# Kernel optimization log

Measured on AMD Instinct MI355X. Metric: run time of the kernel, lower is better.

Reference implementation:

```python
import jax, jax.numpy as jnp
import numpy as np

N, E, B, O = 100000, 1600000, 256, 32
D, H, OD = 128, 128, 32  # node_features, hidden_dim, order_encoding_dim
L = 3  # num_layers


def setup_inputs() -> dict:
    key = jax.random.key(0)
    ks = jax.random.split(key, 32)
    g = lambda k, s, fan: jax.random.normal(k, s, jnp.float32) * (1.0 / np.sqrt(fan))
    inp = {
        'x': jax.random.normal(ks[0], (N, D), jnp.float32),
        'edge_index': jax.random.randint(ks[1], (2, E), 0, N),
        'orders': jax.random.normal(ks[2], (B, O, OD), jnp.float32),
        'batch': jnp.sort(jax.random.randint(ks[3], (N,), 0, B)),
        # GIN layers (input_dim == hidden_dim so all 3 layers stack): MLP = Lin(H,H)->ReLU->Lin(H,H), then BatchNorm1d
        'gW1': g(ks[4], (L, H, H), H), 'gb1': jnp.zeros((L, H)),
        'gW2': g(ks[5], (L, H, H), H), 'gb2': jnp.zeros((L, H)),
        'gamma': jnp.ones((L, H)), 'beta': jnp.zeros((L, H)),
        # order encoder: Lin(OD,H)->ReLU->Lin(H,H)
        'oW1': g(ks[6], (OD, H), OD), 'ob1': jnp.zeros((H,)),
        'oW2': g(ks[7], (H, H), H), 'ob2': jnp.zeros((H,)),
        # score head: Lin(4H,H)->ReLU->Lin(H,H//2)->ReLU->Lin(H//2,1)
        'sW1': g(ks[8], (4 * H, H), 4 * H), 'sb1': jnp.zeros((H,)),
        'sW2': g(ks[9], (H, H // 2), H), 'sb2': jnp.zeros((H // 2,)),
        'sW3': g(ks[10], (H // 2, 1), H // 2), 'sb3': jnp.zeros((1,)),
    }
    return inp


def reference(x, edge_index, orders, batch, gW1, gb1, gW2, gb2, gamma, beta,
              oW1, ob1, oW2, ob2, sW1, sb1, sW2, sb2, sW3, sb3):
    n = x.shape[0]
    src, dst = edge_index[0], edge_index[1]
    h = x
    nl = gW1.shape[0]
    for i in range(nl):  # fixed small layer count
        agg = jax.ops.segment_sum(h[src], dst, num_segments=n)  # sum aggregation
        z = agg + h  # (1 + eps) * x with eps = 0 (GINConv default)
        z = jnp.maximum(z @ gW1[i] + gb1[i], 0) @ gW2[i] + gb2[i]
        mu = z.mean(0)
        var = z.var(0)  # biased var, as torch BN uses for normalization
        z = (z - mu) * jax.lax.rsqrt(var + 1e-5) * gamma[i] + beta[i]
        h = jnp.maximum(z, 0) if i < nl - 1 else z  # dropout inactive (eval)
    b = orders.shape[0]
    cnt = jax.ops.segment_sum(jnp.ones((n,), h.dtype), batch, num_segments=b)
    ssum = jax.ops.segment_sum(h, batch, num_segments=b)
    smean = ssum / jnp.maximum(cnt, 1)[:, None]
    smax = jax.ops.segment_max(h, batch, num_segments=b)
    smax = jnp.where(jnp.isfinite(smax), smax, 0)
    graph = jnp.concatenate([smean, smax, ssum], axis=-1)  # [B, 3H]
    # batched over num_orders (equivalent to the python per-order loop)
    oe = jnp.maximum(orders @ oW1 + ob1, 0) @ oW2 + ob2  # [B, O, H]
    comb = jnp.concatenate(
        [jnp.broadcast_to(graph[:, None, :], (b, orders.shape[1], graph.shape[-1])), oe], axis=-1)
    s = jnp.maximum(comb @ sW1 + sb1, 0)
    s = jnp.maximum(s @ sW2 + sb2, 0)
    s = (s @ sW3 + sb3)[..., 0]  # [B, O]
    return s
```

## Files before the change

### kernel.cpp

```cpp
#include <hip/hip_runtime.h>

static constexpr int NN = 100000;
static constexpr int NE = 1600000;
static constexpr int NB = 256;
static constexpr int NO = 32;
static constexpr int HD = 128;
static constexpr long NH = (long)NN * HD;

static constexpr int BSHIFT = 9;
static constexpr int BSIZE = 1 << BSHIFT;
static constexpr int NBUCK = 256;
static constexpr int BCAP = 10240;
static constexpr int CHUNK = 16384;
static constexpr int NCHUNK = (NE + CHUNK - 1) / CHUNK;
static constexpr int POOL_ROWS = 64;
static constexpr int POOL_GRID = (NN + POOL_ROWS - 1) / POOL_ROWS;
static constexpr int NSUB = 64;
static constexpr int GATHER_GRID = NN / 4;
static constexpr int FL_ROWS = 32;
static constexpr int FL_GRID = (NN + FL_ROWS - 1) / FL_ROWS;

typedef _Float16 f16x8 __attribute__((ext_vector_type(8)));
typedef _Float16 f16x4 __attribute__((ext_vector_type(4)));
typedef _Float16 f16x2 __attribute__((ext_vector_type(2)));
typedef float f32x4 __attribute__((ext_vector_type(4)));

__device__ __forceinline__ unsigned int encf(float f) {
  unsigned int u = __float_as_uint(f);
  return (u & 0x80000000u) ? ~u : (u | 0x80000000u);
}
__device__ __forceinline__ float decf(unsigned int e) {
  return (e & 0x80000000u) ? __uint_as_float(e & 0x7fffffffu) : __uint_as_float(~e);
}

__global__ void bucket_scatter(const int* __restrict__ ei, int* __restrict__ cursor,
                               unsigned int* __restrict__ binned) {
  __shared__ int cnt[NBUCK];
  __shared__ int runbase[NBUCK];
  const int t = threadIdx.x;
  cnt[t] = 0;
  __syncthreads();
  long start = (long)blockIdx.x * CHUNK;
  long end = min((long)NE, start + CHUNK);
  for (long e = start + t; e < end; e += 256)
    atomicAdd(&cnt[ei[NE + e] >> BSHIFT], 1);
  __syncthreads();
  int c = cnt[t];
  runbase[t] = c ? atomicAdd(&cursor[t], c) : 0;
  cnt[t] = 0;
  __syncthreads();
  for (long e = start + t; e < end; e += 256) {
    int d = ei[NE + e], s = ei[e];
    int b = d >> BSHIFT;
    int pos = b * BCAP + runbase[b] + atomicAdd(&cnt[b], 1);
    binned[pos] = ((unsigned int)s << BSHIFT) | (unsigned int)(d & (BSIZE - 1));
  }
}

__global__ void bucket_csr(const unsigned int* __restrict__ binned,
                           const int* __restrict__ cursor,
                           int* __restrict__ rowStart, int* __restrict__ rowEnd,
                           int* __restrict__ col) {
  __shared__ int cnt[BSIZE];
  __shared__ int excl[BSIZE];
  __shared__ int cur[BSIZE];
  __shared__ int part[256];
  const int b = blockIdx.x;
  const int t = threadIdx.x;
  const int lo = b * BCAP;
  const int hi = lo + cursor[b];
  cnt[t] = 0; cnt[t + 256] = 0;
  __syncthreads();
  for (int i = lo + t; i < hi; i += 256)
    atomicAdd(&cnt[binned[i] & (BSIZE - 1)], 1);
  __syncthreads();
  int a0 = cnt[2 * t], a1 = cnt[2 * t + 1];
  int s = a0 + a1;
  part[t] = s;
  __syncthreads();
  for (int off = 1; off < 256; off <<= 1) {
    int u = (t >= off) ? part[t - off] : 0;
    __syncthreads();
    part[t] += u;
    __syncthreads();
  }
  int ebase = part[t] - s;
  excl[2 * t] = ebase;
  excl[2 * t + 1] = ebase + a0;
  __syncthreads();
  const int node0 = b * BSIZE;
  for (int i = t; i < BSIZE; i += 256) {
    int node = node0 + i;
    if (node < NN) {
      rowStart[node] = lo + excl[i];
      rowEnd[node]   = lo + excl[i] + cnt[i];
    }
    cur[i] = lo + excl[i];
  }
  __syncthreads();
  for (int i = lo + t; i < hi; i += 256) {
    unsigned int v = binned[i];
    int pos = atomicAdd(&cur[v & (BSIZE - 1)], 1);
    col[pos] = (int)(v >> BSHIFT);
  }
}

__global__ void f32to16_kernel(const float* __restrict__ in, _Float16* __restrict__ out) {
  long i = (long)(blockIdx.x * 256 + threadIdx.x) * 8;
  if (i >= NH) return;
  float4 a = *reinterpret_cast<const float4*>(in + i);
  float4 b = *reinterpret_cast<const float4*>(in + i + 4);
  f16x8 v;
  v[0] = (_Float16)a.x; v[1] = (_Float16)a.y; v[2] = (_Float16)a.z; v[3] = (_Float16)a.w;
  v[4] = (_Float16)b.x; v[5] = (_Float16)b.y; v[6] = (_Float16)b.z; v[7] = (_Float16)b.w;
  *reinterpret_cast<f16x8*>(out + i) = v;
}

__global__ void pack_w_kernel(const float* __restrict__ gW1, const float* __restrict__ gW2,
                              _Float16* __restrict__ Wp) {
  int tid = blockIdx.x * blockDim.x + threadIdx.x;
  if (tid >= 12288) return;
  int lane = tid & 63;
  int s = (tid >> 6) & 3;
  int t = (tid >> 8) & 7;
  int which = (tid >> 11) & 1;
  int layer = tid >> 12;
  const float* W = (which ? gW2 : gW1) + (long)layer * 128 * 128;
  _Float16* dst = Wp + (long)tid * 8;
  int kbase = s * 32 + ((lane >> 4) << 3);
  int n = t * 16 + (lane & 15);
#pragma unroll
  for (int j = 0; j < 8; ++j) dst[j] = (_Float16)W[(kbase + j) * 128 + n];
}

__global__ void pack_head_kernel(const float* __restrict__ oW1, const float* __restrict__ oW2,
                                 const float* __restrict__ sW1, const float* __restrict__ sW2,
                                 _Float16* __restrict__ dst) {
  int tid = blockIdx.x * blockDim.x + threadIdx.x;
  if (tid >= 5632) return;
  const float* W; int K, N, rowOff;
  int base = tid;
  if (tid < 512)       { W = oW1; K = 32;  N = 128; rowOff = 0;   }
  else if (tid < 2560) { W = oW2; K = 128; N = 128; rowOff = 0;   base = tid - 512; }
  else if (tid < 4608) { W = sW1; K = 128; N = 128; rowOff = 384; base = tid - 2560; }
  else                 { W = sW2; K = 128; N = 64;  rowOff = 0;   base = tid - 4608; }
  int lane = base & 63;
  int fs = base >> 6;
  int NS = K >> 5;
  int s = fs % NS;
  int tt = fs / NS;
  int k = s * 32 + ((lane >> 4) << 3);
  int n = tt * 16 + (lane & 15);
  _Float16* d = dst + (long)tid * 8;
#pragma unroll
  for (int j = 0; j < 8; ++j) d[j] = (_Float16)W[(long)(rowOff + k + j) * N + n];
}

__global__ void gather_kernel(const _Float16* __restrict__ hin, const int* __restrict__ rowStart,
                              const int* __restrict__ rowEnd, const int* __restrict__ col,
                              _Float16* __restrict__ z) {
  const int node = (blockIdx.x * blockDim.x + threadIdx.x) >> 6;
  if (node >= NN) return;
  const int c2 = (threadIdx.x & 63) * 2;
  auto ldh = [&](int n) -> float2 {
    f16x2 h = *reinterpret_cast<const f16x2*>(hin + (long)n * HD + c2);
    return make_float2((float)h[0], (float)h[1]);
  };
  const int lo = rowStart[node];
  const int hi = rowEnd[node];
  float2 acc = ldh(node);
  int j = lo;
  for (; j + 4 <= hi; j += 4) {
    int s0 = col[j], s1 = col[j + 1], s2 = col[j + 2], s3 = col[j + 3];
    float2 v0 = ldh(s0), v1 = ldh(s1), v2 = ldh(s2), v3 = ldh(s3);
    acc.x += (v0.x + v1.x) + (v2.x + v3.x);
    acc.y += (v0.y + v1.y) + (v2.y + v3.y);
  }
  if (j < hi) {
    int last = hi - 1;
    int s0 = col[j];
    int s1 = col[min(j + 1, last)];
    int s2 = col[min(j + 2, last)];
    int s3 = col[min(j + 3, last)];
    float m1 = (j + 1 < hi) ? 1.f : 0.f;
    float m2 = (j + 2 < hi) ? 1.f : 0.f;
    float m3 = (j + 3 < hi) ? 1.f : 0.f;
    float2 v0 = ldh(s0), v1 = ldh(s1), v2 = ldh(s2), v3 = ldh(s3);
    acc.x += v0.x + m1 * v1.x + m2 * v2.x + m3 * v3.x;
    acc.y += v0.y + m1 * v1.y + m2 * v2.y + m3 * v3.y;
  }
  f16x2 o;
  o[0] = (_Float16)acc.x;
  o[1] = (_Float16)acc.y;
  *reinterpret_cast<f16x2*>(z + (long)node * HD + c2) = o;
}

__global__ void __launch_bounds__(128)
fused_layer(const _Float16* __restrict__ Z, const _Float16* __restrict__ Wp,
            const float* __restrict__ b1, const float* __restrict__ b2,
            _Float16* __restrict__ Z2, float* __restrict__ accum2) {
  __shared__ _Float16 Abuf[FL_ROWS * 136];
  __shared__ float red[256];
  const int t = threadIdx.x;
  const int row0 = blockIdx.x * FL_ROWS;
  const int lane = t & 63;
  const int w = t >> 6;
  const int l15 = lane & 15;
  const int kgrp = lane >> 4;

  for (int idx = t; idx < FL_ROWS * 16; idx += 128) {
    int r = idx >> 4;
    int c8 = (idx & 15) * 8;
    int row = row0 + r;
    f16x8 v = {};
    if (row < NN) v = *reinterpret_cast<const f16x8*>(Z + (long)row * HD + c8);
    *reinterpret_cast<f16x8*>(&Abuf[r * 136 + c8]) = v;
  }
  red[t] = 0.f;
  red[t + 128] = 0.f;
  __syncthreads();

  f32x4 acc[8];
  {
    f16x8 af[4];
#pragma unroll
    for (int s = 0; s < 4; ++s)
      af[s] = *reinterpret_cast<const f16x8*>(&Abuf[(w * 16 + l15) * 136 + s * 32 + kgrp * 8]);
    const _Float16* W1p = Wp;
#pragma unroll
    for (int tt = 0; tt < 8; ++tt) {
      float bb = b1[tt * 16 + l15];
      acc[tt] = (f32x4){bb, bb, bb, bb};
#pragma unroll
      for (int s = 0; s < 4; ++s) {
        f16x8 bf = *reinterpret_cast<const f16x8*>(W1p + ((tt * 4 + s) * 64 + lane) * 8);
        acc[tt] = __builtin_amdgcn_mfma_f32_16x16x32_f16(af[s], bf, acc[tt], 0, 0, 0);
      }
    }
  }
#pragma unroll
  for (int tt = 0; tt < 8; ++tt) {
#pragma unroll
    for (int j = 0; j < 4; ++j) {
      float v = fmaxf(acc[tt][j], 0.f);
      Abuf[(w * 16 + kgrp * 4 + j) * 136 + tt * 16 + l15] = (_Float16)v;
    }
  }
  {
    f16x8 af[4];
#pragma unroll
    for (int s = 0; s < 4; ++s)
      af[s] = *reinterpret_cast<const f16x8*>(&Abuf[(w * 16 + l15) * 136 + s * 32 + kgrp * 8]);
    const _Float16* W2p = Wp + 16384;
#pragma unroll
    for (int tt = 0; tt < 8; ++tt) {
      float bb = b2[tt * 16 + l15];
      acc[tt] = (f32x4){bb, bb, bb, bb};
#pragma unroll
      for (int s = 0; s < 4; ++s) {
        f16x8 bf = *reinterpret_cast<const f16x8*>(W2p + ((tt * 4 + s) * 64 + lane) * 8);
        acc[tt] = __builtin_amdgcn_mfma_f32_16x16x32_f16(af[s], bf, acc[tt], 0, 0, 0);
      }
    }
  }
#pragma unroll
  for (int tt = 0; tt < 8; ++tt) {
    int c = tt * 16 + l15;
    float s = 0.f, q = 0.f;
#pragma unroll
    for (int j = 0; j < 4; ++j) {
      int r = row0 + w * 16 + kgrp * 4 + j;
      float v = acc[tt][j];
      if (r < NN) { s += v; q += v * v; }
      Abuf[(w * 16 + kgrp * 4 + j) * 136 + c] = (_Float16)v;
    }
    atomicAdd(&red[c], s);
    atomicAdd(&red[128 + c], q);
  }
  for (int idx = lane; idx < 16 * 16; idx += 64) {
    int r = w * 16 + (idx >> 4);
    int c8 = (idx & 15) * 8;
    int row = row0 + r;
    if (row < NN)
      *reinterpret_cast<f16x8*>(Z2 + (long)row * HD + c8) =
          *reinterpret_cast<const f16x8*>(&Abuf[r * 136 + c8]);
  }
  __syncthreads();
  atomicAdd(&accum2[(blockIdx.x & (NSUB - 1)) * 256 + t], red[t]);
  atomicAdd(&accum2[(blockIdx.x & (NSUB - 1)) * 256 + t + 128], red[t + 128]);
}

__global__ void bn_reduce(float* __restrict__ accum2, const float* __restrict__ gamma,
                          const float* __restrict__ beta, float* __restrict__ scsh) {
  const int c = threadIdx.x;
  float s = 0.f;
  for (int i = 0; i < NSUB; ++i) {
    s += accum2[i * 256 + c];
    accum2[i * 256 + c] = 0.f;
  }
  __shared__ float red[256];
  red[c] = s;
  __syncthreads();
  if (c < 128) {
    const float n = (float)NN;
    float mu = red[c] / n;
    float var = red[128 + c] / n - mu * mu;
    float sc = rsqrtf(var + 1e-5f) * gamma[c];
    scsh[c] = sc;
    scsh[128 + c] = beta[c] - mu * sc;
  }
}

__global__ void bn_apply(const _Float16* __restrict__ z2, const float* __restrict__ scsh,
                         _Float16* __restrict__ hn) {
  long idx = (long)blockIdx.x * 256 + threadIdx.x;
  if (idx >= (long)NN * 16) return;
  int c8 = ((int)idx & 15) * 8;
  float4 sc0 = *reinterpret_cast<const float4*>(scsh + c8);
  float4 sc1 = *reinterpret_cast<const float4*>(scsh + c8 + 4);
  float4 sh0 = *reinterpret_cast<const float4*>(scsh + 128 + c8);
  float4 sh1 = *reinterpret_cast<const float4*>(scsh + 128 + c8 + 4);
  f16x8 v = *reinterpret_cast<const f16x8*>(z2 + idx * 8);
  f16x8 o;
  o[0] = (_Float16)fmaxf(fmaf((float)v[0], sc0.x, sh0.x), 0.f);
  o[1] = (_Float16)fmaxf(fmaf((float)v[1], sc0.y, sh0.y), 0.f);
  o[2] = (_Float16)fmaxf(fmaf((float)v[2], sc0.z, sh0.z), 0.f);
  o[3] = (_Float16)fmaxf(fmaf((float)v[3], sc0.w, sh0.w), 0.f);
  o[4] = (_Float16)fmaxf(fmaf((float)v[4], sc1.x, sh1.x), 0.f);
  o[5] = (_Float16)fmaxf(fmaf((float)v[5], sc1.y, sh1.y), 0.f);
  o[6] = (_Float16)fmaxf(fmaf((float)v[6], sc1.z, sh1.z), 0.f);
  o[7] = (_Float16)fmaxf(fmaf((float)v[7], sc1.w, sh1.w), 0.f);
  *reinterpret_cast<f16x8*>(hn + idx * 8) = o;
}

__global__ void pool_init(float* __restrict__ ssum, unsigned int* __restrict__ smaxU) {
  int i = blockIdx.x * 256 + threadIdx.x;
  ssum[i] = 0.f;
  smaxU[i] = 0x007FFFFFu;
}

__global__ void pool_partial(const _Float16* __restrict__ z2, const float* __restrict__ scsh,
                             const int* __restrict__ batch,
                             float* __restrict__ ssum, unsigned int* __restrict__ smaxU) {
  const int c = threadIdx.x;
  const int row0 = blockIdx.x * POOL_ROWS;
  const int rowEnd = min(row0 + POOL_ROWS, NN);
  const float sc = scsh[c];
  const float sh = scsh[128 + c];

  int curb = batch[row0];
  float s = 0.f, m = -INFINITY;
  for (int row = row0; row < rowEnd; ++row) {
    int b = batch[row];
    if (b != curb) {
      atomicAdd(&ssum[curb * HD + c], s);
      atomicMax(&smaxU[curb * HD + c], encf(m));
      s = 0.f; m = -INFINITY; curb = b;
    }
    float v = fmaf((float)z2[(long)row * HD + c], sc, sh);
    s += v;
    m = fmaxf(m, v);
  }
  atomicAdd(&ssum[curb * HD + c], s);
  atomicMax(&smaxU[curb * HD + c], encf(m));
}

__global__ void pool_gpart(const int* __restrict__ batch, const float* __restrict__ ssum,
                           const unsigned int* __restrict__ smaxU, const float* __restrict__ sW1,
                           const float* __restrict__ sb1, float* __restrict__ gpart) {
  __shared__ float sm[128], sx[128], ss[128];
  const int b = blockIdx.x;
  const int c = threadIdx.x;
  int lo = 0, hi = NN;
  while (lo < hi) { int mid = (lo + hi) >> 1; if (batch[mid] < b) lo = mid + 1; else hi = mid; }
  const int start = lo;
  hi = NN;
  while (lo < hi) { int mid = (lo + hi) >> 1; if (batch[mid] < b + 1) lo = mid + 1; else hi = mid; }
  const int cnt = lo - start;
  float s = ssum[b * HD + c];
  sm[c] = s / fmaxf((float)cnt, 1.f);
  sx[c] = (cnt > 0) ? decf(smaxU[b * HD + c]) : 0.f;
  ss[c] = s;
  __syncthreads();
  float acc = sb1[c];
  for (int k = 0; k < 128; ++k) acc = fmaf(sm[k], sW1[k * 128 + c], acc);
  for (int k = 0; k < 128; ++k) acc = fmaf(sx[k], sW1[(128 + k) * 128 + c], acc);
  for (int k = 0; k < 128; ++k) acc = fmaf(ss[k], sW1[(256 + k) * 128 + c], acc);
  gpart[b * HD + c] = acc;
}

__global__ void __launch_bounds__(128)
head_mfma(const float* __restrict__ orders, const _Float16* __restrict__ Wh,
          const float* __restrict__ ob1, const float* __restrict__ ob2,
          const float* __restrict__ gpart, const float* __restrict__ sb2,
          const float* __restrict__ sW3, const float* __restrict__ sb3,
          float* __restrict__ out) {
  __shared__ _Float16 B1[32 * 136];
  __shared__ _Float16 B2[32 * 136];
  const int t = threadIdx.x;
  const int g = blockIdx.x;
  const int row0 = g * 32;
  const int lane = t & 63;
  const int w = t >> 6;
  const int l15 = lane & 15;
  const int kgrp = lane >> 4;
  const _Float16* oW1p  = Wh;
  const _Float16* oW2p  = Wh + 4096;
  const _Float16* sW1bp = Wh + 20480;
  const _Float16* sW2p  = Wh + 36864;

  for (int idx = t; idx < 32 * 8; idx += 128) {
    int r = idx >> 3;
    int c4 = (idx & 7) * 4;
    float4 v = *reinterpret_cast<const float4*>(orders + (long)(row0 + r) * 32 + c4);
    f16x4 h;
    h[0] = (_Float16)v.x; h[1] = (_Float16)v.y; h[2] = (_Float16)v.z; h[3] = (_Float16)v.w;
    *reinterpret_cast<f16x4*>(&B1[r * 136 + c4]) = h;
  }
  __syncthreads();

  f32x4 acc[8];
  {
    f16x8 a0 = *reinterpret_cast<const f16x8*>(&B1[(w * 16 + l15) * 136 + kgrp * 8]);
#pragma unroll
    for (int tt = 0; tt < 8; ++tt) {
      float bb = ob1[tt * 16 + l15];
      acc[tt] = (f32x4){bb, bb, bb, bb};
      f16x8 bf = *reinterpret_cast<const f16x8*>(oW1p + (tt * 64 + lane) * 8);
      acc[tt] = __builtin_amdgcn_mfma_f32_16x16x32_f16(a0, bf, acc[tt], 0, 0, 0);
    }
#pragma unroll
    for (int tt = 0; tt < 8; ++tt)
#pragma unroll
      for (int j = 0; j < 4; ++j)
        B2[(w * 16 + kgrp * 4 + j) * 136 + tt * 16 + l15] = (_Float16)fmaxf(acc[tt][j], 0.f);
  }
  {
    f16x8 af[4];
#pragma unroll
    for (int s = 0; s < 4; ++s)
      af[s] = *reinterpret_cast<const f16x8*>(&B2[(w * 16 + l15) * 136 + s * 32 + kgrp * 8]);
#pragma unroll
    for (int tt = 0; tt < 8; ++tt) {
      float bb = ob2[tt * 16 + l15];
      acc[tt] = (f32x4){bb, bb, bb, bb};
#pragma unroll
      for (int s = 0; s < 4; ++s) {
        f16x8 bf = *reinterpret_cast<const f16x8*>(oW2p + ((tt * 4 + s) * 64 + lane) * 8);
        acc[tt] = __builtin_amdgcn_mfma_f32_16x16x32_f16(af[s], bf, acc[tt], 0, 0, 0);
      }
    }
#pragma unroll
    for (int tt = 0; tt < 8; ++tt)
#pragma unroll
      for (int j = 0; j < 4; ++j)
        B1[(w * 16 + kgrp * 4 + j) * 136 + tt * 16 + l15] = (_Float16)acc[tt][j];
  }
  {
    f16x8 af[4];
#pragma unroll
    for (int s = 0; s < 4; ++s)
      af[s] = *reinterpret_cast<const f16x8*>(&B1[(w * 16 + l15) * 136 + s * 32 + kgrp * 8]);
#pragma unroll
    for (int tt = 0; tt < 8; ++tt) {
      acc[tt] = (f32x4){0.f, 0.f, 0.f, 0.f};
#pragma unroll
      for (int s = 0; s < 4; ++s) {
        f16x8 bf = *reinterpret_cast<const f16x8*>(sW1bp + ((tt * 4 + s) * 64 + lane) * 8);
        acc[tt] = __builtin_amdgcn_mfma_f32_16x16x32_f16(af[s], bf, acc[tt], 0, 0, 0);
      }
    }
#pragma unroll
    for (int tt = 0; tt < 8; ++tt) {
      int c = tt * 16 + l15;
      float gp = gpart[g * HD + c];
#pragma unroll
      for (int j = 0; j < 4; ++j)
        B2[(w * 16 + kgrp * 4 + j) * 136 + c] = (_Float16)fmaxf(acc[tt][j] + gp, 0.f);
    }
  }
  {
    f16x8 af[4];
#pragma unroll
    for (int s = 0; s < 4; ++s)
      af[s] = *reinterpret_cast<const f16x8*>(&B2[(w * 16 + l15) * 136 + s * 32 + kgrp * 8]);
#pragma unroll
    for (int tt = 0; tt < 4; ++tt) {
      float bb = sb2[tt * 16 + l15];
      acc[tt] = (f32x4){bb, bb, bb, bb};
#pragma unroll
      for (int s = 0; s < 4; ++s) {
        f16x8 bf = *reinterpret_cast<const f16x8*>(sW2p + ((tt * 4 + s) * 64 + lane) * 8);
        acc[tt] = __builtin_amdgcn_mfma_f32_16x16x32_f16(af[s], bf, acc[tt], 0, 0, 0);
      }
    }
    float rsum[4] = {0.f, 0.f, 0.f, 0.f};
#pragma unroll
    for (int tt = 0; tt < 4; ++tt) {
      float wv = sW3[tt * 16 + l15];
#pragma unroll
      for (int j = 0; j < 4; ++j)
        rsum[j] = fmaf(fmaxf(acc[tt][j], 0.f), wv, rsum[j]);
    }
#pragma unroll
    for (int j = 0; j < 4; ++j) {
      rsum[j] += __shfl_xor(rsum[j], 1);
      rsum[j] += __shfl_xor(rsum[j], 2);
      rsum[j] += __shfl_xor(rsum[j], 4);
      rsum[j] += __shfl_xor(rsum[j], 8);
    }
    if (l15 == 0) {
      float b3 = sb3[0];
#pragma unroll
      for (int j = 0; j < 4; ++j)
        out[row0 + w * 16 + kgrp * 4 + j] = rsum[j] + b3;
    }
  }
}

extern "C" void kernel_launch(void* const* d_in, const int* in_sizes, int n_in,
                              void* d_out, int out_size, void* d_ws, size_t ws_size,
                              hipStream_t stream) {
  const float* x      = (const float*)d_in[0];
  const int*   ei     = (const int*)d_in[1];
  const float* orders = (const float*)d_in[2];
  const int*   batch  = (const int*)d_in[3];
  const float* gW1    = (const float*)d_in[4];
  const float* gb1    = (const float*)d_in[5];
  const float* gW2    = (const float*)d_in[6];
  const float* gb2    = (const float*)d_in[7];
  const float* gamma  = (const float*)d_in[8];
  const float* beta   = (const float*)d_in[9];
  const float* oW1    = (const float*)d_in[10];
  const float* ob1    = (const float*)d_in[11];
  const float* oW2    = (const float*)d_in[12];
  const float* ob2    = (const float*)d_in[13];
  const float* sW1    = (const float*)d_in[14];
  const float* sb1    = (const float*)d_in[15];
  const float* sW2    = (const float*)d_in[16];
  const float* sb2    = (const float*)d_in[17];
  const float* sW3    = (const float*)d_in[18];
  const float* sb3    = (const float*)d_in[19];
  float* out = (float*)d_out;

  char* ws = (char*)d_ws;
  _Float16* xh    = (_Float16*)ws;
  _Float16* bufAh = xh + NH;
  _Float16* bufCh = bufAh + NH;
  float* accum2 = (float*)(bufCh + NH);
  float* scsh   = accum2 + NSUB * 256;
  float* ssum   = scsh + 256;
  unsigned int* smaxU = (unsigned int*)(ssum + NB * HD);
  float* gpart = (float*)(smaxU + NB * HD);
  int* rowStart = (int*)(gpart + NB * HD);
  int* rowEnd   = rowStart + NN;
  int* col      = rowEnd + NN;
  unsigned int* binned = (unsigned int*)(col + NBUCK * BCAP);
  int* cursor = (int*)(binned + NBUCK * BCAP);
  _Float16* Wp  = (_Float16*)(cursor + NBUCK);
  _Float16* Wh  = Wp + 3 * 32768;

  hipMemsetAsync(cursor, 0, NBUCK * sizeof(int), stream);
  bucket_scatter<<<NCHUNK, 256, 0, stream>>>(ei, cursor, binned);
  bucket_csr<<<NBUCK, 256, 0, stream>>>(binned, cursor, rowStart, rowEnd, col);

  pack_w_kernel<<<48, 256, 0, stream>>>(gW1, gW2, Wp);
  pack_head_kernel<<<22, 256, 0, stream>>>(oW1, oW2, sW1, sW2, Wh);
  f32to16_kernel<<<(int)(NH / 8 + 255) / 256, 256, 0, stream>>>(x, xh);
  hipMemsetAsync(accum2, 0, NSUB * 256 * sizeof(float), stream);

  const int BA_GRID = (int)((NN * 16 + 255) / 256);
  for (int l = 0; l < 3; ++l) {
    gather_kernel<<<GATHER_GRID, 256, 0, stream>>>(xh, rowStart, rowEnd, col, bufAh);
    fused_layer<<<FL_GRID, 128, 0, stream>>>(
        bufAh, Wp + (long)l * 32768, gb1 + l * 128, gb2 + l * 128, bufCh, accum2);
    bn_reduce<<<1, 256, 0, stream>>>(accum2, gamma + l * 128, beta + l * 128, scsh);
    if (l < 2) bn_apply<<<BA_GRID, 256, 0, stream>>>(bufCh, scsh, xh);
  }

  pool_init<<<128, 256, 0, stream>>>(ssum, smaxU);
  pool_partial<<<POOL_GRID, 128, 0, stream>>>(bufCh, scsh, batch, ssum, smaxU);
  pool_gpart<<<NB, 128, 0, stream>>>(batch, ssum, smaxU, sW1, sb1, gpart);

  head_mfma<<<NB, 128, 0, stream>>>(orders, Wh, ob1, ob2, gpart, sb2, sW3, sb3, out);
}
```

Baseline: 535.8 us.

## Replace atomic BN and pooling reductions with per-block partials and sort CSR columns

BatchNorm statistics now use wave shuffles and per-block partial sums written to a buffer, followed by a multi-block tree reduction, instead of shared and global float atomics. Pooling is split into fixed per-graph chunks whose partial sum and max are combined in pool_gpart, which removes the encoded atomicMax and the init kernel. A new kernel insertion-sorts each node's neighbor list, which makes the summation order deterministic and may improve gather locality. It also drops bounds checks because NN divides by the row tile. The trade is an extra sort pass and a larger partial buffer in exchange for fewer contended atomics and reproducible results.

```diff
diff --git a/kernel.cpp b/kernel.cpp
--- a/kernel.cpp
+++ b/kernel.cpp
@@ -13,25 +13,15 @@
 static constexpr int BCAP = 10240;
 static constexpr int CHUNK = 16384;
 static constexpr int NCHUNK = (NE + CHUNK - 1) / CHUNK;
-static constexpr int POOL_ROWS = 64;
-static constexpr int POOL_GRID = (NN + POOL_ROWS - 1) / POOL_ROWS;
-static constexpr int NSUB = 64;
+static constexpr int NPCH = 8;
 static constexpr int GATHER_GRID = NN / 4;
 static constexpr int FL_ROWS = 32;
-static constexpr int FL_GRID = (NN + FL_ROWS - 1) / FL_ROWS;
+static constexpr int FL_GRID = NN / FL_ROWS;
 
 typedef _Float16 f16x8 __attribute__((ext_vector_type(8)));
 typedef _Float16 f16x4 __attribute__((ext_vector_type(4)));
 typedef _Float16 f16x2 __attribute__((ext_vector_type(2)));
 typedef float f32x4 __attribute__((ext_vector_type(4)));
-
-__device__ __forceinline__ unsigned int encf(float f) {
-  unsigned int u = __float_as_uint(f);
-  return (u & 0x80000000u) ? ~u : (u | 0x80000000u);
-}
-__device__ __forceinline__ float decf(unsigned int e) {
-  return (e & 0x80000000u) ? __uint_as_float(e & 0x7fffffffu) : __uint_as_float(~e);
-}
 
 __global__ void bucket_scatter(const int* __restrict__ ei, int* __restrict__ cursor,
                                unsigned int* __restrict__ binned) {
@@ -102,6 +92,19 @@
     unsigned int v = binned[i];
     int pos = atomicAdd(&cur[v & (BSIZE - 1)], 1);
     col[pos] = (int)(v >> BSHIFT);
+  }
+}
+
+__global__ void sort_cols(const int* __restrict__ rowStart, const int* __restrict__ rowEnd,
+                          int* __restrict__ col) {
+  int n = blockIdx.x * 256 + threadIdx.x;
+  if (n >= NN) return;
+  int lo = rowStart[n], hi = rowEnd[n];
+  for (int i = lo + 1; i < hi; ++i) {
+    int key = col[i];
+    int j = i - 1;
+    while (j >= lo && col[j] > key) { col[j + 1] = col[j]; --j; }
+    col[j + 1] = key;
   }
 }
 
@@ -198,9 +201,9 @@
 __global__ void __launch_bounds__(128)
 fused_layer(const _Float16* __restrict__ Z, const _Float16* __restrict__ Wp,
             const float* __restrict__ b1, const float* __restrict__ b2,
-            _Float16* __restrict__ Z2, float* __restrict__ accum2) {
+            _Float16* __restrict__ Z2, float* __restrict__ partial) {
   __shared__ _Float16 Abuf[FL_ROWS * 136];
-  __shared__ float red[256];
+  __shared__ float ps[256], pq[256];
   const int t = threadIdx.x;
   const int row0 = blockIdx.x * FL_ROWS;
   const int lane = t & 63;
@@ -211,13 +214,9 @@
   for (int idx = t; idx < FL_ROWS * 16; idx += 128) {
     int r = idx >> 4;
     int c8 = (idx & 15) * 8;
-    int row = row0 + r;
-    f16x8 v = {};
-    if (row < NN) v = *reinterpret_cast<const f16x8*>(Z + (long)row * HD + c8);
+    f16x8 v = *reinterpret_cast<const f16x8*>(Z + (long)(row0 + r) * HD + c8);
     *reinterpret_cast<f16x8*>(&Abuf[r * 136 + c8]) = v;
   }
-  red[t] = 0.f;
-  red[t + 128] = 0.f;
   __syncthreads();
 
   f32x4 acc[8];
@@ -269,42 +268,47 @@
     float s = 0.f, q = 0.f;
 #pragma unroll
     for (int j = 0; j < 4; ++j) {
-      int r = row0 + w * 16 + kgrp * 4 + j;
       float v = acc[tt][j];
-      if (r < NN) { s += v; q += v * v; }
+      s += v; q += v * v;
       Abuf[(w * 16 + kgrp * 4 + j) * 136 + c] = (_Float16)v;
     }
-    atomicAdd(&red[c], s);
-    atomicAdd(&red[128 + c], q);
+    s += __shfl_xor(s, 16); s += __shfl_xor(s, 32);
+    q += __shfl_xor(q, 16); q += __shfl_xor(q, 32);
+    if (kgrp == 0) { ps[w * 128 + c] = s; pq[w * 128 + c] = q; }
   }
   for (int idx = lane; idx < 16 * 16; idx += 64) {
     int r = w * 16 + (idx >> 4);
     int c8 = (idx & 15) * 8;
-    int row = row0 + r;
-    if (row < NN)
-      *reinterpret_cast<f16x8*>(Z2 + (long)row * HD + c8) =
-          *reinterpret_cast<const f16x8*>(&Abuf[r * 136 + c8]);
-  }
-  __syncthreads();
-  atomicAdd(&accum2[(blockIdx.x & (NSUB - 1)) * 256 + t], red[t]);
-  atomicAdd(&accum2[(blockIdx.x & (NSUB - 1)) * 256 + t + 128], red[t + 128]);
-}
-
-__global__ void bn_reduce(float* __restrict__ accum2, const float* __restrict__ gamma,
+    *reinterpret_cast<f16x8*>(Z2 + (long)(row0 + r) * HD + c8) =
+        *reinterpret_cast<const f16x8*>(&Abuf[r * 136 + c8]);
+  }
+  __syncthreads();
+  if (t < 128) {
+    partial[(long)blockIdx.x * 256 + t]       = ps[t] + ps[128 + t];
+    partial[(long)blockIdx.x * 256 + 128 + t] = pq[t] + pq[128 + t];
+  }
+}
+
+__global__ void bn_reduce(const float* __restrict__ partial, const float* __restrict__ gamma,
                           const float* __restrict__ beta, float* __restrict__ scsh) {
-  const int c = threadIdx.x;
+  __shared__ float red[256];
+  const int c = blockIdx.x;
+  const int t = threadIdx.x;
+  const int ch = (t < 128) ? c : (128 + c);
+  const int j = t & 127;
   float s = 0.f;
-  for (int i = 0; i < NSUB; ++i) {
-    s += accum2[i * 256 + c];
-    accum2[i * 256 + c] = 0.f;
-  }
-  __shared__ float red[256];
-  red[c] = s;
-  __syncthreads();
-  if (c < 128) {
+  for (int blk = j; blk < FL_GRID; blk += 128)
+    s += partial[(long)blk * 256 + ch];
+  red[t] = s;
+  __syncthreads();
+  for (int off = 64; off > 0; off >>= 1) {
+    if ((t & 127) < off) red[t] += red[t + off];
+    __syncthreads();
+  }
+  if (t == 0) {
     const float n = (float)NN;
-    float mu = red[c] / n;
-    float var = red[128 + c] / n - mu * mu;
+    float mu = red[0] / n;
+    float var = red[128] / n - mu * mu;
     float sc = rsqrtf(var + 1e-5f) * gamma[c];
     scsh[c] = sc;
     scsh[128 + c] = beta[c] - mu * sc;
@@ -333,40 +337,36 @@
   *reinterpret_cast<f16x8*>(hn + idx * 8) = o;
 }
 
-__global__ void pool_init(float* __restrict__ ssum, unsigned int* __restrict__ smaxU) {
-  int i = blockIdx.x * 256 + threadIdx.x;
-  ssum[i] = 0.f;
-  smaxU[i] = 0x007FFFFFu;
-}
-
 __global__ void pool_partial(const _Float16* __restrict__ z2, const float* __restrict__ scsh,
                              const int* __restrict__ batch,
-                             float* __restrict__ ssum, unsigned int* __restrict__ smaxU) {
+                             float* __restrict__ pps, float* __restrict__ ppm) {
+  const int b = blockIdx.x >> 3;
+  const int k = blockIdx.x & 7;
   const int c = threadIdx.x;
-  const int row0 = blockIdx.x * POOL_ROWS;
-  const int rowEnd = min(row0 + POOL_ROWS, NN);
+  int lo = 0, hi = NN;
+  while (lo < hi) { int mid = (lo + hi) >> 1; if (batch[mid] < b) lo = mid + 1; else hi = mid; }
+  const int start = lo;
+  hi = NN;
+  while (lo < hi) { int mid = (lo + hi) >> 1; if (batch[mid] < b + 1) lo = mid + 1; else hi = mid; }
+  const int end = lo;
+  const int cnt = end - start;
+  const int chunk = (cnt + NPCH - 1) >> 3;
+  const int r0 = start + k * chunk;
+  const int r1 = min(r0 + chunk, end);
   const float sc = scsh[c];
   const float sh = scsh[128 + c];
-
-  int curb = batch[row0];
   float s = 0.f, m = -INFINITY;
-  for (int row = row0; row < rowEnd; ++row) {
-    int b = batch[row];
-    if (b != curb) {
-      atomicAdd(&ssum[curb * HD + c], s);
-      atomicMax(&smaxU[curb * HD + c], encf(m));
-      s = 0.f; m = -INFINITY; curb = b;
-    }
+  for (int row = r0; row < r1; ++row) {
     float v = fmaf((float)z2[(long)row * HD + c], sc, sh);
     s += v;
     m = fmaxf(m, v);
   }
-  atomicAdd(&ssum[curb * HD + c], s);
-  atomicMax(&smaxU[curb * HD + c], encf(m));
-}
-
-__global__ void pool_gpart(const int* __restrict__ batch, const float* __restrict__ ssum,
-                           const unsigned int* __restrict__ smaxU, const float* __restrict__ sW1,
+  pps[(long)blockIdx.x * 128 + c] = s;
+  ppm[(long)blockIdx.x * 128 + c] = m;
+}
+
+__global__ void pool_gpart(const int* __restrict__ batch, const float* __restrict__ pps,
+                           const float* __restrict__ ppm, const float* __restrict__ sW1,
                            const float* __restrict__ sb1, float* __restrict__ gpart) {
   __shared__ float sm[128], sx[128], ss[128];
   const int b = blockIdx.x;
@@ -377,9 +377,14 @@
   hi = NN;
   while (lo < hi) { int mid = (lo + hi) >> 1; if (batch[mid] < b + 1) lo = mid + 1; else hi = mid; }
   const int cnt = lo - start;
-  float s = ssum[b * HD + c];
+  float s = 0.f, m = -INFINITY;
+#pragma unroll
+  for (int k = 0; k < NPCH; ++k) {
+    s += pps[(long)(b * NPCH + k) * 128 + c];
+    m = fmaxf(m, ppm[(long)(b * NPCH + k) * 128 + c]);
+  }
   sm[c] = s / fmaxf((float)cnt, 1.f);
-  sx[c] = (cnt > 0) ? decf(smaxU[b * HD + c]) : 0.f;
+  sx[c] = (cnt > 0) ? m : 0.f;
   ss[c] = s;
   __syncthreads();
   float acc = sb1[c];
@@ -547,11 +552,11 @@
   _Float16* xh    = (_Float16*)ws;
   _Float16* bufAh = xh + NH;
   _Float16* bufCh = bufAh + NH;
-  float* accum2 = (float*)(bufCh + NH);
-  float* scsh   = accum2 + NSUB * 256;
-  float* ssum   = scsh + 256;
-  unsigned int* smaxU = (unsigned int*)(ssum + NB * HD);
-  float* gpart = (float*)(smaxU + NB * HD);
+  float* partial = (float*)(bufCh + NH);
+  float* scsh    = partial + (long)FL_GRID * 256;
+  float* pps     = scsh + 256;
+  float* ppm     = pps + NB * NPCH * 128;
+  float* gpart   = ppm + NB * NPCH * 128;
   int* rowStart = (int*)(gpart + NB * HD);
   int* rowEnd   = rowStart + NN;
   int* col      = rowEnd + NN;
@@ -563,24 +568,23 @@
   hipMemsetAsync(cursor, 0, NBUCK * sizeof(int), stream);
   bucket_scatter<<<NCHUNK, 256, 0, stream>>>(ei, cursor, binned);
   bucket_csr<<<NBUCK, 256, 0, stream>>>(binned, cursor, rowStart, rowEnd, col);
+  sort_cols<<<(NN + 255) / 256, 256, 0, stream>>>(rowStart, rowEnd, col);
 
   pack_w_kernel<<<48, 256, 0, stream>>>(gW1, gW2, Wp);
   pack_head_kernel<<<22, 256, 0, stream>>>(oW1, oW2, sW1, sW2, Wh);
   f32to16_kernel<<<(int)(NH / 8 + 255) / 256, 256, 0, stream>>>(x, xh);
-  hipMemsetAsync(accum2, 0, NSUB * 256 * sizeof(float), stream);
 
   const int BA_GRID = (int)((NN * 16 + 255) / 256);
   for (int l = 0; l < 3; ++l) {
     gather_kernel<<<GATHER_GRID, 256, 0, stream>>>(xh, rowStart, rowEnd, col, bufAh);
     fused_layer<<<FL_GRID, 128, 0, stream>>>(
-        bufAh, Wp + (long)l * 32768, gb1 + l * 128, gb2 + l * 128, bufCh, accum2);
-    bn_reduce<<<1, 256, 0, stream>>>(accum2, gamma + l * 128, beta + l * 128, scsh);
+        bufAh, Wp + (long)l * 32768, gb1 + l * 128, gb2 + l * 128, bufCh, partial);
+    bn_reduce<<<128, 256, 0, stream>>>(partial, gamma + l * 128, beta + l * 128, scsh);
     if (l < 2) bn_apply<<<BA_GRID, 256, 0, stream>>>(bufCh, scsh, xh);
   }
 
-  pool_init<<<128, 256, 0, stream>>>(ssum, smaxU);
-  pool_partial<<<POOL_GRID, 128, 0, stream>>>(bufCh, scsh, batch, ssum, smaxU);
-  pool_gpart<<<NB, 128, 0, stream>>>(batch, ssum, smaxU, sW1, sb1, gpart);
+  pool_partial<<<NB * NPCH, 128, 0, stream>>>(bufCh, scsh, batch, pps, ppm);
+  pool_gpart<<<NB, 128, 0, stream>>>(batch, pps, ppm, sW1, sb1, gpart);
 
   head_mfma<<<NB, 128, 0, stream>>>(orders, Wh, ob1, ob2, gpart, sb2, sW3, sb3, out);
 }
```

Result: slower. 580.1 us (+8.3%).
